# Kernel tuning notes

Hardware: AMD Instinct MI355X
Metric: run time of the kernel (lower is better)

The kernel has to match this reference:

```python
import jax, jax.numpy as jnp
import numpy as np
from jax import lax

B, C_IN, T = 64, 40, 8192

def conv1d(x, w, b):
    # x: [B,C,T], w: [O,I,K] (torch Conv1d layout), stride 2, VALID padding
    y = lax.conv_general_dilated(x, w, window_strides=(2,), padding='VALID',
                                 dimension_numbers=('NCH', 'OIH', 'NCH'))
    return y + b[None, :, None]

def avgpool2(x):
    # AvgPool1d(kernel=2, stride=2): pairwise mean, drop trailing odd element
    t2 = x.shape[-1] // 2
    return x[..., :2 * t2].reshape(x.shape[0], x.shape[1], t2, 2).mean(-1)

def setup_inputs():
    key = jax.random.key(0)
    ks = jax.random.split(key, 24)
    def w_init(k, shape, fan_in):
        return jax.random.normal(k, shape, jnp.float32) * (1.0 / np.sqrt(fan_in))
    inp = {}
    inp['x_input'] = jax.random.normal(ks[0], (B, C_IN, T), jnp.float32)
    # per-sample valid lengths in [2048, 8192] so the deep strided stack leaves >=1 frame
    inp['len_mask'] = 2048 + jax.random.randint(ks[1], (B,), 0, T - 2048 + 1, dtype=jnp.int32)
    convs = [(96, C_IN, 10), (96, 96, 5), (96, 96, 5), (96, 96, 5), (96, 96, 5), (96, 96, 5), (128, 96, 3)]
    for i, (o, ci, k) in enumerate(convs):
        inp[f'w{i+1}'] = w_init(ks[2 + 2 * i], (o, ci, k), ci * k)
        inp[f'b{i+1}'] = jnp.zeros((o,), jnp.float32)
    lins = [(128, 128), (64, 128), (5, 64)]
    for i, (o, ci) in enumerate(lins):
        inp[f'lw{i+1}'] = w_init(ks[16 + 2 * i], (o, ci), ci)
        inp[f'lb{i+1}'] = jnp.zeros((o,), jnp.float32)
    return inp

def reference(x_input, len_mask, w1, b1, w2, b2, w3, b3, w4, b4, w5, b5, w6, b6, w7, b7,
              lw1, lb1, lw2, lb2, lw3, lb3):
    # Batched masked equivalent of the per-sample ragged loop: for VALID stride-2 convs,
    # output position j depends only on inputs < valid length when j < valid out-length,
    # so we run batched convs on padded input and track per-sample valid lengths.
    Lv = len_mask.astype(jnp.int32)
    x = jax.nn.relu(conv1d(x_input, w1, b1)); Lv = (Lv - 10) // 2 + 1
    x = jax.nn.relu(conv1d(x, w2, b2));       Lv = (Lv - 5) // 2 + 1
    x = jax.nn.relu(conv1d(x, w3, b3));       Lv = (Lv - 5) // 2 + 1
    # cnn_1d_top (dropout in eval mode = identity)
    x = conv1d(x, w4, b4);        Lv = (Lv - 5) // 2 + 1
    x = jax.nn.relu(avgpool2(x)); Lv = Lv // 2
    x = conv1d(x, w5, b5);        Lv = (Lv - 5) // 2 + 1
    x = jax.nn.relu(avgpool2(x)); Lv = Lv // 2
    x = jax.nn.relu(conv1d(x, w6, b6)); Lv = (Lv - 5) // 2 + 1
    x = jax.nn.relu(conv1d(x, w7, b7)); Lv = (Lv - 3) // 2 + 1
    # AdaptiveMaxPool1d(1) over each sample's valid region
    mask = jnp.arange(x.shape[-1])[None, :] < Lv[:, None]          # [B, T_out]
    x = jnp.max(jnp.where(mask[:, None, :], x, -jnp.inf), axis=-1)  # [B, 128]
    # out1_top MLP head
    h = jax.nn.relu(x @ lw1.T + lb1)
    h = jax.nn.relu(h @ lw2.T + lb2)
    return h @ lw3.T + lb3
```

## Files before the change

### kernel.cpp

```cpp
#include <hip/hip_runtime.h>
#include <hip/hip_bf16.h>
#include <math.h>


typedef __attribute__((ext_vector_type(8))) _Float16 f16x8;
typedef __attribute__((ext_vector_type(4))) float f32x4;

__device__ __forceinline__ unsigned short f2h_bits(float f) {
    union { _Float16 h; unsigned short u; } cv;
    cv.h = (_Float16)f;
    return cv.u;
}

template<int KEFF, int CI, int NBLK, bool IN_FP32, bool RELU, bool OUT_F16,
         bool POOL, int PIPE, int PHASES>
__global__ __launch_bounds__(512, 2)
void conv_nb(const unsigned short* __restrict__ xh,
             const unsigned short* __restrict__ wpk,
             const float* __restrict__ bias,
             unsigned short* __restrict__ yh,
             float* __restrict__ yf,
             int Tin, int Tout)
{
    constexpr int CO    = 96;
    constexpr int NTHR  = 512;
    constexpr int GTOT  = CI * KEFF;
    constexpr int STEPS = (GTOT + 31) / 32;
    constexpr int SH    = STEPS / PHASES;
    constexpr int CIH   = CI / PHASES;
    constexpr int RD    = NBLK + KEFF / 2;
    constexpr int NTW   = NBLK / 64;
    constexpr int TOTH  = CIH * RD;
    constexpr int NIT   = (TOTH + NTHR - 1) / NTHR;
    constexpr int PH    = (32 % KEFF == 0) ? 1 : (((32 * 3) % KEFF == 0) ? 3 : 5);
    constexpr int PERRD = (32 * PH / KEFF) * RD;

    __shared__ unsigned int Bs[TOTH];

    const int tid  = threadIdx.x;
    const int lane = tid & 63;
    const int wave = tid >> 6;
    const int mg   = wave & 1;
    const int tg   = wave >> 1;
    const int quad = lane >> 4;
    const int l16  = lane & 15;
    const int wc0  = tg * (NBLK / 4);

    const int nT = (Tout + NBLK - 1) / NBLK;
    const int b  = blockIdx.x / nT;
    const int t0 = (blockIdx.x % nT) * NBLK;

    const float* xf = (const float*)xh;
    const unsigned int* xb = (const unsigned int*)xh + (((size_t)b * CI * Tin) >> 1);
    const int rowd = Tin >> 1;

    auto stageB = [&](int ph) {
        const int ci0 = ph * CIH;
        #pragma unroll
        for (int it = 0; it < NIT; ++it) {
            int i = tid + it * NTHR;
            if (i < TOTH) {
                int r = (unsigned)i / (unsigned)RD, d = i - r * RD;
                unsigned int v;
                if (IN_FP32) {
                    int e = 2 * (t0 + d);
                    if (e > Tin - 2) e = Tin - 2;
                    const float* src = xf + ((size_t)b * CI + ci0 + r) * Tin + e;
                    float2 w = *(const float2*)src;
                    v = (unsigned int)f2h_bits(w.x) | ((unsigned int)f2h_bits(w.y) << 16);
                } else {
                    int dd = t0 + d;
                    if (dd > rowd - 1) dd = rowd - 1;
                    v = *(xb + (size_t)(ci0 + r) * rowd + dd);
                }
                Bs[i] = v;
            }
        }
    };

    int offb[PH][4];
    #pragma unroll
    for (int ph = 0; ph < PH; ++ph)
        #pragma unroll
        for (int p = 0; p < 4; ++p) {
            int g = 32 * ph + quad * 8 + 2 * p;
            unsigned ci = (unsigned)g / (unsigned)KEFF;
            unsigned dwo = ((unsigned)g - ci * (unsigned)KEFF) >> 1;
            offb[ph][p] = (int)ci * RD + wc0 + l16 + (int)dwo;
        }

    f32x4 acc[3][NTW];
    #pragma unroll
    for (int mt = 0; mt < 3; ++mt)
        #pragma unroll
        for (int nt = 0; nt < NTW; ++nt) acc[mt][nt] = (f32x4)0.f;

    union BvU { unsigned int u[4]; f16x8 v; };

    auto load_step = [&](int sg, int sl, BvU (&Bv)[NTW], f16x8 (&Ah)[3], f16x8 (&Al)[3]) {
        if (32 * (sg + 1) <= GTOT) {
            #pragma unroll
            for (int nt = 0; nt < NTW; ++nt)
                #pragma unroll
                for (int p = 0; p < 4; ++p)
                    Bv[nt].u[p] = Bs[offb[sl % PH][p] + (sl / PH) * PERRD + nt * 16];
        } else {
            #pragma unroll
            for (int nt = 0; nt < NTW; ++nt)
                #pragma unroll
                for (int p = 0; p < 4; ++p) {
                    int g = 32 * sg + quad * 8 + 2 * p;
                    if (g > GTOT - 2) g = GTOT - 2;
                    unsigned ci = (unsigned)g / (unsigned)KEFF;
                    unsigned dwo = ((unsigned)g - ci * (unsigned)KEFF) >> 1;
                    Bv[nt].u[p] = Bs[(int)ci * RD + wc0 + l16 + (int)dwo + nt * 16];
                }
        }
        const unsigned short* ap = wpk + (size_t)sg * 6144 + (size_t)(mg * 3) * 512
                                 + (size_t)lane * 8;
        #pragma unroll
        for (int mt = 0; mt < 3; ++mt) {
            Ah[mt] = *(const f16x8*)(ap + mt * 512);
            Al[mt] = *(const f16x8*)(ap + 3072 + mt * 512);
        }
    };
    auto mfma_step = [&](BvU (&Bv)[NTW], f16x8 (&Ah)[3], f16x8 (&Al)[3]) {
        #pragma unroll
        for (int mt = 0; mt < 3; ++mt)
            #pragma unroll
            for (int nt = 0; nt < NTW; ++nt)
                acc[mt][nt] = __builtin_amdgcn_mfma_f32_16x16x32_f16(Ah[mt], Bv[nt].v, acc[mt][nt], 0, 0, 0);
        #pragma unroll
        for (int mt = 0; mt < 3; ++mt)
            #pragma unroll
            for (int nt = 0; nt < NTW; ++nt)
                acc[mt][nt] = __builtin_amdgcn_mfma_f32_16x16x32_f16(Al[mt], Bv[nt].v, acc[mt][nt], 0, 0, 0);
    };

    #pragma unroll
    for (int ph2 = 0; ph2 < PHASES; ++ph2) {
        if (ph2 > 0) __syncthreads();
        stageB(ph2);
        __syncthreads();

        if (PIPE == 0) {
            #pragma unroll
            for (int s2 = 0; s2 < SH; ++s2) {
                BvU Bv[NTW];
                f16x8 Ah[3], Al[3];
                load_step(ph2 * SH + s2, s2, Bv, Ah, Al);
                mfma_step(Bv, Ah, Al);
            }
        } else {
            BvU  Bv0[NTW], Bv1[NTW];
            f16x8 Ah0[3], Al0[3], Ah1[3], Al1[3];

            load_step(ph2 * SH, 0, Bv0, Ah0, Al0);
            #pragma unroll
            for (int s2 = 0; s2 < SH; ++s2) {
                if (s2 + 1 < SH) {
                    if (((s2 + 1) & 1) == 0) load_step(ph2 * SH + s2 + 1, s2 + 1, Bv0, Ah0, Al0);
                    else                     load_step(ph2 * SH + s2 + 1, s2 + 1, Bv1, Ah1, Al1);
                }
                __builtin_amdgcn_sched_barrier(0);
                __builtin_amdgcn_s_setprio(1);
                if ((s2 & 1) == 0) mfma_step(Bv0, Ah0, Al0);
                else               mfma_step(Bv1, Ah1, Al1);
                __builtin_amdgcn_s_setprio(0);
                __builtin_amdgcn_sched_barrier(0);
            }
        }
    }

    #pragma unroll
    for (int mt = 0; mt < 3; ++mt) {
        #pragma unroll
        for (int r = 0; r < 4; ++r) {
            int o = (mg * 3 + mt) * 16 + quad * 4 + r;
            float bv = bias[o];
            #pragma unroll
            for (int nt = 0; nt < NTW; ++nt) {
                int t = t0 + wc0 + nt * 16 + l16;
                float v = acc[mt][nt][r] + bv;
                if (RELU) v = fmaxf(v, 0.f);
                if (POOL) {
                    float sum = v + __shfl_xor(v, 1, 64);
                    if ((lane & 1) == 0 && t + 1 < Tout) {
                        float pr = fmaxf(0.5f * sum, 0.f);
                        size_t pidx = ((size_t)b * CO + o) * (Tout >> 1) + (t >> 1);
                        if (OUT_F16) yh[pidx] = f2h_bits(pr);
                        else         yf[pidx] = pr;
                    }
                } else if (OUT_F16) {
                    unsigned int h = f2h_bits(v);
                    unsigned int hp = (unsigned int)__shfl_xor((int)h, 1, 64);
                    if ((lane & 1) == 0 && t + 1 < Tout) {
                        size_t base = ((size_t)b * CO + o) * Tout + t;
                        *(unsigned int*)(yh + base) = h | (hp << 16);
                    }
                } else if (t < Tout) {
                    yf[((size_t)b * CO + o) * Tout + t] = v;
                }
            }
        }
    }
}

__global__ __launch_bounds__(512, 2)
void tail3(const unsigned short* __restrict__ y4h,
           const unsigned short* __restrict__ wpk5,
           const float* __restrict__ b5,
           const float* __restrict__ w6r, const float* __restrict__ b6,
           const float* __restrict__ w7r, const float* __restrict__ b7,
           const int* __restrict__ lens,
           const float* __restrict__ lw1, const float* __restrict__ lb1,
           const float* __restrict__ lw2, const float* __restrict__ lb2,
           const float* __restrict__ lw3, const float* __restrict__ lb3,
           float* __restrict__ out)
{
    constexpr int RD  = 131;
    constexpr int TOT = 96 * RD;
    constexpr int NIT = (TOT + 511) / 512;
    constexpr int PERRD = 16 * RD;

    __shared__ __align__(16) unsigned int smem[TOT];
    float* const y5s  = (float*)smem;
    float* const y6s  = (float*)smem + 96 * 62;
    float* const s7   = (float*)smem + 96 * 62 + 96 * 29 + 8;
    float* const feat = s7 + 128 * 14;
    float* const h1   = feat + 128;
    float* const h2   = h1 + 128;

    const int tid  = threadIdx.x;
    const int lane = tid & 63;
    const int wave = tid >> 6;
    const int mg   = wave & 1;
    const int tg   = wave >> 1;
    const int quad = lane >> 4;
    const int l16  = lane & 15;
    const int wc0  = tg * 32;
    const int b    = blockIdx.x;

    const unsigned int* xb = (const unsigned int*)y4h + (size_t)b * 96 * 127;
    #pragma unroll
    for (int it = 0; it < NIT; ++it) {
        int i = tid + it * 512;
        if (i < TOT) {
            int r = (unsigned)i / (unsigned)RD, d = i - r * RD;
            if (d > 126) d = 126;
            smem[i] = xb[(size_t)r * 127 + d];
        }
    }
    __syncthreads();

    int offb[3][4];
    #pragma unroll
    for (int ph = 0; ph < 3; ++ph)
        #pragma unroll
        for (int p = 0; p < 4; ++p) {
            int g = 32 * ph + quad * 8 + 2 * p;
            int ci = g / 6, dwo = (g - ci * 6) >> 1;
            offb[ph][p] = ci * RD + wc0 + l16 + dwo;
        }

    f32x4 acc[3][2];
    #pragma unroll
    for (int mt = 0; mt < 3; ++mt)
        #pragma unroll
        for (int nt = 0; nt < 2; ++nt) acc[mt][nt] = (f32x4)0.f;

    union BvU { unsigned int u[4]; f16x8 v; };
    auto load_step = [&](int s, BvU (&Bv)[2], f16x8 (&Ah)[3], f16x8 (&Al)[3]) {
        #pragma unroll
        for (int nt = 0; nt < 2; ++nt)
            #pragma unroll
            for (int p = 0; p < 4; ++p)
                Bv[nt].u[p] = smem[offb[s % 3][p] + (s / 3) * PERRD + nt * 16];
        const unsigned short* ap = wpk5 + (size_t)s * 6144 + (size_t)(mg * 3) * 512
                                 + (size_t)lane * 8;
        #pragma unroll
        for (int mt = 0; mt < 3; ++mt) {
            Ah[mt] = *(const f16x8*)(ap + mt * 512);
            Al[mt] = *(const f16x8*)(ap + 3072 + mt * 512);
        }
    };
    auto mfma_step = [&](BvU (&Bv)[2], f16x8 (&Ah)[3], f16x8 (&Al)[3]) {
        #pragma unroll
        for (int mt = 0; mt < 3; ++mt)
            #pragma unroll
            for (int nt = 0; nt < 2; ++nt)
                acc[mt][nt] = __builtin_amdgcn_mfma_f32_16x16x32_f16(Ah[mt], Bv[nt].v, acc[mt][nt], 0, 0, 0);
        #pragma unroll
        for (int mt = 0; mt < 3; ++mt)
            #pragma unroll
            for (int nt = 0; nt < 2; ++nt)
                acc[mt][nt] = __builtin_amdgcn_mfma_f32_16x16x32_f16(Al[mt], Bv[nt].v, acc[mt][nt], 0, 0, 0);
    };

    {
        BvU  Bv0[2], Bv1[2];
        f16x8 Ah0[3], Al0[3], Ah1[3], Al1[3];
        load_step(0, Bv0, Ah0, Al0);
        #pragma unroll
        for (int s = 0; s < 18; ++s) {
            if (s + 1 < 18) {
                if (((s + 1) & 1) == 0) load_step(s + 1, Bv0, Ah0, Al0);
                else                    load_step(s + 1, Bv1, Ah1, Al1);
            }
            __builtin_amdgcn_sched_barrier(0);
            __builtin_amdgcn_s_setprio(1);
            if ((s & 1) == 0) mfma_step(Bv0, Ah0, Al0);
            else              mfma_step(Bv1, Ah1, Al1);
            __builtin_amdgcn_s_setprio(0);
            __builtin_amdgcn_sched_barrier(0);
        }
    }

    __syncthreads();

    #pragma unroll
    for (int mt = 0; mt < 3; ++mt) {
        #pragma unroll
        for (int r = 0; r < 4; ++r) {
            int o = (mg * 3 + mt) * 16 + quad * 4 + r;
            float bv = b5[o];
            #pragma unroll
            for (int nt = 0; nt < 2; ++nt) {
                int t = wc0 + nt * 16 + l16;
                float v = acc[mt][nt][r] + bv;
                float sum = v + __shfl_xor(v, 1, 64);
                if ((lane & 1) == 0 && t + 1 < 125)
                    y5s[o * 62 + (t >> 1)] = fmaxf(0.5f * sum, 0.f);
            }
        }
    }
    __syncthreads();

    {
        const int half = lane >> 5;
        const int t = lane & 31;
        const int o0 = wave * 12 + half * 6;
        if (t < 29) {
            float a6[6];
            #pragma unroll
            for (int oo = 0; oo < 6; oo++) a6[oo] = 0.f;
            for (int ci = 0; ci < 96; ci++) {
                float xr[5];
                #pragma unroll
                for (int k = 0; k < 5; k++) xr[k] = y5s[ci * 62 + 2 * t + k];
                #pragma unroll
                for (int k = 0; k < 5; k++) {
                    const float* wp = w6r + (ci * 5 + k) * 96 + o0;
                    #pragma unroll
                    for (int oo = 0; oo < 6; oo++)
                        a6[oo] = fmaf(wp[oo], xr[k], a6[oo]);
                }
            }
            #pragma unroll
            for (int oo = 0; oo < 6; oo++)
                y6s[(o0 + oo) * 29 + t] = fmaxf(a6[oo] + b6[o0 + oo], 0.f);
        }
    }
    __syncthreads();

    {
        const int sub = lane >> 4;
        const int tl  = lane & 15;
        float a7[16];
        #pragma unroll
        for (int oo = 0; oo < 16; oo++) a7[oo] = 0.f;
        const int ci0 = sub * 24;
        for (int ci = ci0; ci < ci0 + 24; ci++) {
            float xr[3];
            #pragma unroll
            for (int k = 0; k < 3; k++) xr[k] = y6s[ci * 29 + 2 * tl + k];
            #pragma unroll
            for (int k = 0; k < 3; k++) {
                const float* wp = w7r + (ci * 3 + k) * 128 + wave * 16;
                #pragma unroll
                for (int oo = 0; oo < 16; oo++)
                    a7[oo] = fmaf(wp[oo], xr[k], a7[oo]);
            }
        }
        #pragma unroll
        for (int oo = 0; oo < 16; oo++) {
            float v = a7[oo];
            v += __shfl_xor(v, 16, 64);
            v += __shfl_xor(v, 32, 64);
            if (sub == 0 && tl < 14) {
                int o = wave * 16 + oo;
                s7[o * 14 + tl] = fmaxf(v + b7[o], 0.f);
            }
        }
    }
    __syncthreads();

    if (tid < 128) {
        int L = lens[b];
        L = (L - 10) / 2 + 1;
        L = (L - 5) / 2 + 1;
        L = (L - 5) / 2 + 1;
        L = (L - 5) / 2 + 1;
        L = L / 2;
        L = (L - 5) / 2 + 1;
        L = L / 2;
        L = (L - 5) / 2 + 1;
        L = (L - 3) / 2 + 1;
        float m = -INFINITY;
        for (int t = 0; t < L; t++) m = fmaxf(m, s7[tid * 14 + t]);
        feat[tid] = m;
    }
    __syncthreads();

    if (tid < 128) {
        float s = lb1[tid];
        for (int i = 0; i < 128; i++) s = fmaf(lw1[tid * 128 + i], feat[i], s);
        h1[tid] = fmaxf(s, 0.f);
    }
    __syncthreads();
    if (tid < 64) {
        float s = lb2[tid];
        for (int i = 0; i < 128; i++) s = fmaf(lw2[tid * 128 + i], h1[i], s);
        h2[tid] = fmaxf(s, 0.f);
    }
    __syncthreads();
    if (tid < 5) {
        float s = lb3[tid];
        for (int i = 0; i < 64; i++) s = fmaf(lw3[tid * 64 + i], h2[i], s);
        out[b * 5 + tid] = s;
    }
}

__device__ __forceinline__ void repack_img(const float* __restrict__ w,
                                           unsigned short* __restrict__ wpk,
                                           int idx, int KP, int KW, int CI)
{
    int j = idx & 7, lane = (idx >> 3) & 63, g = idx >> 9;
    int c = g / 24, r = g % 24;
    int mt = r % 6, sh = r / 6;
    int half = sh & 1, s = sh >> 1;
    int S  = c * 2 + s;
    int kg = S * 32 + (lane >> 4) * 8 + j;
    int o  = mt * 16 + (lane & 15);
    int ci = kg / KP, k = kg - ci * KP;
    float val = (ci < CI && k < KW) ? w[((size_t)o * CI + ci) * KW + k] : 0.f;
    _Float16 hh = (_Float16)val;
    union { _Float16 h; unsigned short u; } cv;
    cv.h = (half == 0) ? hh : (_Float16)(val - (float)hh);
    wpk[idx] = cv.u;
}
__device__ __forceinline__ void repack_okc(const float* __restrict__ w,
                                           float* __restrict__ wr,
                                           int idx, int CI, int K, int CO)
{
    int o = idx % CO; int rem = idx / CO; int k = rem % K; int ci = rem / K;
    wr[idx] = w[((size_t)o * CI + ci) * K + k];
}

__global__ void repack_all(const float* w1, const float* w2, const float* w3,
                           const float* w4, const float* w5, const float* w6,
                           const float* w7,
                           unsigned short* p1, unsigned short* p2,
                           unsigned short* p3, unsigned short* p4,
                           unsigned short* p5, float* r6, float* r7)
{
    int idx = blockIdx.x * 256 + threadIdx.x;
    if (idx < 79872)  { repack_img(w1, p1, idx, 10, 10, 40); return; }
    idx -= 79872;
    if (idx < 110592) { repack_img(w2, p2, idx, 6, 5, 96); return; }
    idx -= 110592;
    if (idx < 110592) { repack_img(w3, p3, idx, 6, 5, 96); return; }
    idx -= 110592;
    if (idx < 110592) { repack_img(w4, p4, idx, 6, 5, 96); return; }
    idx -= 110592;
    if (idx < 110592) { repack_img(w5, p5, idx, 6, 5, 96); return; }
    idx -= 110592;
    if (idx < 46080)  { repack_okc(w6, r6, idx, 96, 5, 96); return; }
    idx -= 46080;
    if (idx < 36864)  { repack_okc(w7, r7, idx, 96, 3, 128); return; }
}

extern "C" void kernel_launch(void* const* d_in, const int* in_sizes, int n_in,
                              void* d_out, int out_size, void* d_ws, size_t ws_size,
                              hipStream_t stream)
{
    const float* x    = (const float*)d_in[0];
    const int*   lens = (const int*)  d_in[1];
    const float* w1 = (const float*)d_in[2];   const float* b1 = (const float*)d_in[3];
    const float* w2 = (const float*)d_in[4];   const float* b2 = (const float*)d_in[5];
    const float* w3 = (const float*)d_in[6];   const float* b3 = (const float*)d_in[7];
    const float* w4 = (const float*)d_in[8];   const float* b4 = (const float*)d_in[9];
    const float* w5 = (const float*)d_in[10];  const float* b5 = (const float*)d_in[11];
    const float* w6 = (const float*)d_in[12];  const float* b6 = (const float*)d_in[13];
    const float* w7 = (const float*)d_in[14];  const float* b7 = (const float*)d_in[15];
    const float* lw1 = (const float*)d_in[16]; const float* lb1 = (const float*)d_in[17];
    const float* lw2 = (const float*)d_in[18]; const float* lb2 = (const float*)d_in[19];
    const float* lw3 = (const float*)d_in[20]; const float* lb3 = (const float*)d_in[21];
    float* out = (float*)d_out;
    char*  W   = (char*)d_ws;

    size_t off = 0;
    auto take = [&](size_t bytes) {
        size_t o = off; off = (off + bytes + 255) & ~(size_t)255; return o;
    };
    size_t o_y3h = take(((size_t)64 * 96 * 1020 + 2048) * 2);
    size_t o_y4h = take(((size_t)64 * 96 * 254 + 2048) * 2);
    size_t o_wp1 = take((size_t)79872 * 2);
    size_t o_wp2 = take((size_t)110592 * 2);
    size_t o_wp3 = take((size_t)110592 * 2);
    size_t o_wp4 = take((size_t)110592 * 2);
    size_t o_wp5 = take((size_t)110592 * 2);
    size_t o_w6r = take((size_t)46080 * 4);
    size_t o_w7r = take((size_t)36864 * 4);
    size_t persist = off;

    auto chunk_bytes = [&](int Bc) -> size_t {
        size_t s = 0;
        s += ((size_t)Bc * 96 * 4092 + 2048) * 2 + 256;
        s += ((size_t)Bc * 96 * 2044 + 2048) * 2 + 256;
        return s;
    };
    int Bc = 64;
    while (Bc > 1 && persist + chunk_bytes(Bc) > ws_size) Bc >>= 1;
    size_t o_y1h = take(((size_t)Bc * 96 * 4092 + 2048) * 2);
    size_t o_y2h = take(((size_t)Bc * 96 * 2044 + 2048) * 2);

    auto US = [&](size_t o) { return (unsigned short*)(W + o); };
    auto FP = [&](size_t o) { return (float*)(W + o); };

    repack_all<<<dim3((605184 + 255) / 256), 256, 0, stream>>>(
        w1, w2, w3, w4, w5, w6, w7,
        US(o_wp1), US(o_wp2), US(o_wp3), US(o_wp4), US(o_wp5),
        FP(o_w6r), FP(o_w7r));

    const int nchunks = 64 / Bc;
    for (int c = 0; c < nchunks; c++) {
        const float* xc = x + (size_t)c * Bc * 40 * 8192;

        conv_nb<10, 40, 256, true, true, true, false, 0, 1><<<dim3(Bc * 16), 512, 0, stream>>>(
            (const unsigned short*)xc, US(o_wp1), b1, US(o_y1h), nullptr, 8192, 4092);
        conv_nb< 6, 96, 128, false, true, true, false, 1, 1><<<dim3(Bc * 16), 512, 0, stream>>>(
            US(o_y1h), US(o_wp2), b2, US(o_y2h), nullptr, 4092, 2044);
        unsigned short* y3h_c = US(o_y3h) + (size_t)c * Bc * 96 * 1020;
        conv_nb< 6, 96, 128, false, true, true, false, 1, 1><<<dim3(Bc * 8), 512, 0, stream>>>(
            US(o_y2h), US(o_wp3), b3, y3h_c, nullptr, 2044, 1020);
    }

    conv_nb<6, 96, 64, false, false, true, true, 1, 1><<<dim3(64 * 8), 512, 0, stream>>>(
        US(o_y3h), US(o_wp4), b4, US(o_y4h), nullptr, 1020, 508);

    tail3<<<dim3(64), 512, 0, stream>>>(
        US(o_y4h), US(o_wp5), b5, FP(o_w6r), b6, FP(o_w7r), b7,
        lens, lw1, lb1, lw2, lb2, lw3, lb3, out);
}
```

Before: 386.3 us.

## Drop MFMA double-buffering and vectorize tail conv and MLP weight loads

Removes the explicit two-stage register double-buffering, sched barriers and priority hints from the conv5 MFMA loop, folding load and compute into one step and leaving scheduling to the compiler. The conv6 and conv7 scalar FMA loops now unroll four input channels at a time and fetch weights as float2/float4 vectors, and the three MLP layers read weight rows as float4. The goal is fewer global load instructions and more memory-level parallelism in the tail of the fused kernel. Removing the manual pipeline may expose load latency in the MFMA loop, and the extra unrolling raises register pressure.

```diff
diff --git a/kernel.cpp b/kernel.cpp
--- a/kernel.cpp
+++ b/kernel.cpp
@@ -270,7 +270,11 @@
         for (int nt = 0; nt < 2; ++nt) acc[mt][nt] = (f32x4)0.f;
 
     union BvU { unsigned int u[4]; f16x8 v; };
-    auto load_step = [&](int s, BvU (&Bv)[2], f16x8 (&Ah)[3], f16x8 (&Al)[3]) {
+
+    #pragma unroll
+    for (int s = 0; s < 18; ++s) {
+        BvU Bv[2];
+        f16x8 Ah[3], Al[3];
         #pragma unroll
         for (int nt = 0; nt < 2; ++nt)
             #pragma unroll
@@ -283,8 +287,6 @@
             Ah[mt] = *(const f16x8*)(ap + mt * 512);
             Al[mt] = *(const f16x8*)(ap + 3072 + mt * 512);
         }
-    };
-    auto mfma_step = [&](BvU (&Bv)[2], f16x8 (&Ah)[3], f16x8 (&Al)[3]) {
         #pragma unroll
         for (int mt = 0; mt < 3; ++mt)
             #pragma unroll
@@ -295,25 +297,6 @@
             #pragma unroll
             for (int nt = 0; nt < 2; ++nt)
                 acc[mt][nt] = __builtin_amdgcn_mfma_f32_16x16x32_f16(Al[mt], Bv[nt].v, acc[mt][nt], 0, 0, 0);
-    };
-
-    {
-        BvU  Bv0[2], Bv1[2];
-        f16x8 Ah0[3], Al0[3], Ah1[3], Al1[3];
-        load_step(0, Bv0, Ah0, Al0);
-        #pragma unroll
-        for (int s = 0; s < 18; ++s) {
-            if (s + 1 < 18) {
-                if (((s + 1) & 1) == 0) load_step(s + 1, Bv0, Ah0, Al0);
-                else                    load_step(s + 1, Bv1, Ah1, Al1);
-            }
-            __builtin_amdgcn_sched_barrier(0);
-            __builtin_amdgcn_s_setprio(1);
-            if ((s & 1) == 0) mfma_step(Bv0, Ah0, Al0);
-            else              mfma_step(Bv1, Ah1, Al1);
-            __builtin_amdgcn_s_setprio(0);
-            __builtin_amdgcn_sched_barrier(0);
-        }
     }
 
     __syncthreads();
@@ -344,17 +327,31 @@
             float a6[6];
             #pragma unroll
             for (int oo = 0; oo < 6; oo++) a6[oo] = 0.f;
-            for (int ci = 0; ci < 96; ci++) {
-                float xr[5];
-                #pragma unroll
-                for (int k = 0; k < 5; k++) xr[k] = y5s[ci * 62 + 2 * t + k];
-                #pragma unroll
-                for (int k = 0; k < 5; k++) {
-                    const float* wp = w6r + (ci * 5 + k) * 96 + o0;
+            for (int ci = 0; ci < 96; ci += 4) {
+                float xr[4][5];
+                #pragma unroll
+                for (int cc = 0; cc < 4; cc++)
                     #pragma unroll
-                    for (int oo = 0; oo < 6; oo++)
-                        a6[oo] = fmaf(wp[oo], xr[k], a6[oo]);
-                }
+                    for (int k = 0; k < 5; k++)
+                        xr[cc][k] = y5s[(ci + cc) * 62 + 2 * t + k];
+                float2 wv[4][5][3];
+                #pragma unroll
+                for (int cc = 0; cc < 4; cc++)
+                    #pragma unroll
+                    for (int k = 0; k < 5; k++) {
+                        const float2* wp = (const float2*)(w6r + ((ci + cc) * 5 + k) * 96 + o0);
+                        #pragma unroll
+                        for (int p = 0; p < 3; p++) wv[cc][k][p] = wp[p];
+                    }
+                #pragma unroll
+                for (int cc = 0; cc < 4; cc++)
+                    #pragma unroll
+                    for (int k = 0; k < 5; k++)
+                        #pragma unroll
+                        for (int p = 0; p < 3; p++) {
+                            a6[2 * p]     = fmaf(wv[cc][k][p].x, xr[cc][k], a6[2 * p]);
+                            a6[2 * p + 1] = fmaf(wv[cc][k][p].y, xr[cc][k], a6[2 * p + 1]);
+                        }
             }
             #pragma unroll
             for (int oo = 0; oo < 6; oo++)
@@ -370,17 +367,33 @@
         #pragma unroll
         for (int oo = 0; oo < 16; oo++) a7[oo] = 0.f;
         const int ci0 = sub * 24;
-        for (int ci = ci0; ci < ci0 + 24; ci++) {
-            float xr[3];
-            #pragma unroll
-            for (int k = 0; k < 3; k++) xr[k] = y6s[ci * 29 + 2 * tl + k];
-            #pragma unroll
-            for (int k = 0; k < 3; k++) {
-                const float* wp = w7r + (ci * 3 + k) * 128 + wave * 16;
-                #pragma unroll
-                for (int oo = 0; oo < 16; oo++)
-                    a7[oo] = fmaf(wp[oo], xr[k], a7[oo]);
-            }
+        for (int ci = ci0; ci < ci0 + 24; ci += 4) {
+            float xr[4][3];
+            #pragma unroll
+            for (int cc = 0; cc < 4; cc++)
+                #pragma unroll
+                for (int k = 0; k < 3; k++)
+                    xr[cc][k] = y6s[(ci + cc) * 29 + 2 * tl + k];
+            float4 wv[4][3][4];
+            #pragma unroll
+            for (int cc = 0; cc < 4; cc++)
+                #pragma unroll
+                for (int k = 0; k < 3; k++) {
+                    const float4* wp = (const float4*)(w7r + ((ci + cc) * 3 + k) * 128 + wave * 16);
+                    #pragma unroll
+                    for (int p = 0; p < 4; p++) wv[cc][k][p] = wp[p];
+                }
+            #pragma unroll
+            for (int cc = 0; cc < 4; cc++)
+                #pragma unroll
+                for (int k = 0; k < 3; k++)
+                    #pragma unroll
+                    for (int p = 0; p < 4; p++) {
+                        a7[4 * p]     = fmaf(wv[cc][k][p].x, xr[cc][k], a7[4 * p]);
+                        a7[4 * p + 1] = fmaf(wv[cc][k][p].y, xr[cc][k], a7[4 * p + 1]);
+                        a7[4 * p + 2] = fmaf(wv[cc][k][p].z, xr[cc][k], a7[4 * p + 2]);
+                        a7[4 * p + 3] = fmaf(wv[cc][k][p].w, xr[cc][k], a7[4 * p + 3]);
+                    }
         }
         #pragma unroll
         for (int oo = 0; oo < 16; oo++) {
@@ -414,19 +427,43 @@
 
     if (tid < 128) {
         float s = lb1[tid];
-        for (int i = 0; i < 128; i++) s = fmaf(lw1[tid * 128 + i], feat[i], s);
+        const float4* wv = (const float4*)(lw1 + (size_t)tid * 128);
+        #pragma unroll
+        for (int i = 0; i < 32; i++) {
+            float4 w4 = wv[i];
+            s = fmaf(w4.x, feat[4 * i],     s);
+            s = fmaf(w4.y, feat[4 * i + 1], s);
+            s = fmaf(w4.z, feat[4 * i + 2], s);
+            s = fmaf(w4.w, feat[4 * i + 3], s);
+        }
         h1[tid] = fmaxf(s, 0.f);
     }
     __syncthreads();
     if (tid < 64) {
         float s = lb2[tid];
-        for (int i = 0; i < 128; i++) s = fmaf(lw2[tid * 128 + i], h1[i], s);
+        const float4* wv = (const float4*)(lw2 + (size_t)tid * 128);
+        #pragma unroll
+        for (int i = 0; i < 32; i++) {
+            float4 w4 = wv[i];
+            s = fmaf(w4.x, h1[4 * i],     s);
+            s = fmaf(w4.y, h1[4 * i + 1], s);
+            s = fmaf(w4.z, h1[4 * i + 2], s);
+            s = fmaf(w4.w, h1[4 * i + 3], s);
+        }
         h2[tid] = fmaxf(s, 0.f);
     }
     __syncthreads();
     if (tid < 5) {
         float s = lb3[tid];
-        for (int i = 0; i < 64; i++) s = fmaf(lw3[tid * 64 + i], h2[i], s);
+        const float4* wv = (const float4*)(lw3 + (size_t)tid * 64);
+        #pragma unroll
+        for (int i = 0; i < 16; i++) {
+            float4 w4 = wv[i];
+            s = fmaf(w4.x, h2[4 * i],     s);
+            s = fmaf(w4.y, h2[4 * i + 1], s);
+            s = fmaf(w4.z, h2[4 * i + 2], s);
+            s = fmaf(w4.w, h2[4 * i + 3], s);
+        }
         out[b * 5 + tid] = s;
     }
 }
```

Result: no change. 389.7 us (+0.9%).
